# Kernel optimization log

Measured on AMD Instinct MI355X. Metric: run time of the kernel, lower is better.

The kernel has to match this reference:

```python
import jax, jax.numpy as jnp
import numpy as np

D_MODEL = 768
D_POS = 64
NHEAD = 12
D_FF = 3072
HEAD_DIM = D_MODEL // NHEAD
LN_EPS = 1e-5


def _layer_norm(x, gamma, beta):
    mu = jnp.mean(x, axis=-1, keepdims=True)
    var = jnp.var(x, axis=-1, keepdims=True)
    return (x - mu) * jax.lax.rsqrt(var + LN_EPS) * gamma + beta


def setup_inputs() -> dict:
    key = jax.random.key(0)
    ks = jax.random.split(key, 16)
    L, N = 256, 4
    s = 0.02
    return {
        "src": jax.random.normal(ks[0], (L, N, D_MODEL), jnp.float32),
        "pos": jax.random.normal(ks[1], (N, L, L, D_POS), jnp.float32),
        "q_w": jax.random.normal(ks[2], (D_MODEL, D_MODEL), jnp.float32) * s,
        "q_b": jnp.zeros((D_MODEL,), jnp.float32),
        "k_w": jax.random.normal(ks[3], (D_MODEL, D_MODEL), jnp.float32) * s,
        "k_b": jnp.zeros((D_MODEL,), jnp.float32),
        "v_w": jax.random.normal(ks[4], (D_MODEL, D_MODEL), jnp.float32) * s,
        "v_b": jnp.zeros((D_MODEL,), jnp.float32),
        "p_w": jax.random.normal(ks[5], (D_MODEL, D_POS), jnp.float32) * s,
        "p_b": jnp.zeros((D_MODEL,), jnp.float32),
        "out_w": jax.random.normal(ks[6], (D_MODEL, D_MODEL), jnp.float32) * s,
        "out_b": jnp.zeros((D_MODEL,), jnp.float32),
        "lin1_w": jax.random.normal(ks[7], (D_FF, D_MODEL), jnp.float32) * s,
        "lin1_b": jnp.zeros((D_FF,), jnp.float32),
        "lin2_w": jax.random.normal(ks[8], (D_MODEL, D_FF), jnp.float32) * s,
        "lin2_b": jnp.zeros((D_MODEL,), jnp.float32),
        "n1_g": jnp.ones((D_MODEL,), jnp.float32),
        "n1_b": jnp.zeros((D_MODEL,), jnp.float32),
        "n2_g": jnp.ones((D_MODEL,), jnp.float32),
        "n2_b": jnp.zeros((D_MODEL,), jnp.float32),
    }


def reference(src, pos, q_w, q_b, k_w, k_b, v_w, v_b, p_w, p_b,
              out_w, out_b, lin1_w, lin1_b, lin2_w, lin2_b,
              n1_g, n1_b, n2_g, n2_b):
    L, N, E = src.shape
    H, hd = NHEAD, HEAD_DIM
    scaling = float(hd) ** -0.5

    # projections (F.linear: x @ W.T + b)
    q = (src @ q_w.T + q_b).reshape(L, N, H, hd).transpose(1, 2, 0, 3) * scaling  # (N,H,L,hd)
    k = (src @ k_w.T + k_b).reshape(L, N, H, hd).transpose(1, 2, 0, 3)            # (N,H,L,hd)
    v = (src @ v_w.T + v_b).reshape(L, N, H, hd).transpose(1, 2, 0, 3)            # (N,H,L,hd)
    p = (pos @ p_w.T + p_b).reshape(N, L, L, H, hd)                               # (N,L,L,H,hd)

    # content-content + content-position scores
    scores = jnp.einsum('nhid,nhjd->nhij', q, k) \
           + jnp.einsum('nhid,nijhd->nhij', q, p)                                 # (N,H,L,L)
    attn = jax.nn.softmax(scores, axis=-1)

    ctx = jnp.einsum('nhij,nhjd->nhid', attn, v)          # (N,H,L,hd)
    ctx = ctx.transpose(2, 0, 1, 3).reshape(L, N, E)      # (L,N,E)
    attn_out = ctx @ out_w.T + out_b

    x = _layer_norm(src + attn_out, n1_g, n1_b)
    ff = jax.nn.gelu(x @ lin1_w.T + lin1_b, approximate=False) @ lin2_w.T + lin2_b
    x = _layer_norm(x + ff, n2_g, n2_b)
    return x
```

## Files before the change

### kernel.cpp

```cpp
#include <hip/hip_runtime.h>
#include <hip/hip_bf16.h>
#include <math.h>

typedef __hip_bfloat16 bf16;
typedef unsigned short u16;
typedef __attribute__((ext_vector_type(8))) short bf16x8;
typedef __attribute__((ext_vector_type(4))) float f32x4;

#define L_SEQ 256
#define NB 4
#define EMB 768
#define NH 12
#define DFF 3072
#define HD 64

__device__ __forceinline__ float ldE(const void* p, size_t i, int f32) {
    return f32 ? ((const float*)p)[i] : __bfloat162float(((const bf16*)p)[i]);
}
__device__ __forceinline__ float b2f(u16 v) { return __uint_as_float(((unsigned)v) << 16); }
__device__ __forceinline__ u16 f2b(float v) {
    bf16 h = __float2bfloat16(v);
    return *(u16*)&h;
}

__global__ void detect_kernel(const void* __restrict__ src, int* __restrict__ flagp) {
    __shared__ int cnt[256];
    int t = threadIdx.x;
    unsigned w = ((const unsigned*)src)[t];
    unsigned e = ((w & 0xFFFFu) >> 7) & 0xFFu;
    cnt[t] = (e >= 0xC3u) ? 1 : 0;
    __syncthreads();
    for (int off = 128; off; off >>= 1) {
        if (t < off) cnt[t] += cnt[t + off];
        __syncthreads();
    }
    if (t == 0) *flagp = (cnt[0] > 8) ? 1 : 0;
}

__device__ __forceinline__ void cvt8(u16* dst, const void* s, size_t off, int f32) {
    if (f32) {
        const float* sf = (const float*)s + off;
        #pragma unroll
        for (int t = 0; t < 8; ++t) dst[t] = f2b(sf[t]);
    } else {
        *(uint4*)dst = *(const uint4*)((const u16*)s + off);
    }
}

__global__ void pack_all(u16* __restrict__ xb, u16* __restrict__ wqkv,
                         u16* __restrict__ owb, u16* __restrict__ l1b,
                         u16* __restrict__ l2b, float* __restrict__ biasf,
                         const void* src, const void* qw, const void* kw, const void* vw,
                         const void* ow, const void* l1w, const void* l2w,
                         const void* qb, const void* kb, const void* vb,
                         const void* ob, const void* b1, const void* b2,
                         const int* __restrict__ flagp) {
    const int f32 = *flagp;
    int b = blockIdx.x;
    if (b >= 3840) {
        int o = (b - 3840) * 256 + threadIdx.x;
        if (o >= 6912) return;
        float v;
        if (o < 768)       v = ldE(qb, o, f32);
        else if (o < 1536) v = ldE(kb, o - 768, f32);
        else if (o < 2304) v = ldE(vb, o - 1536, f32);
        else if (o < 3072) v = ldE(ob, o - 2304, f32);
        else if (o < 6144) v = ldE(b1, o - 3072, f32);
        else               v = ldE(b2, o - 6144, f32);
        biasf[o] = v;
        return;
    }
    int gid = b * 256 + threadIdx.x;
    u16 tmp[8];
    if (gid < 98304) {
        size_t idx = (size_t)gid * 8;
        cvt8(tmp, src, idx, f32);
        *(uint4*)(xb + idx) = *(uint4*)tmp;
    } else if (gid < 319488) {
        size_t idx = (size_t)(gid - 98304) * 8;
        int r = (int)(idx / EMB);
        const void* s;
        size_t off;
        if (r < EMB)          { s = qw; off = idx; }
        else if (r < 2 * EMB) { s = kw; off = idx - (size_t)EMB * EMB; }
        else                  { s = vw; off = idx - (size_t)2 * EMB * EMB; }
        cvt8(tmp, s, off, f32);
        *(uint4*)(wqkv + idx) = *(uint4*)tmp;
    } else if (gid < 393216) {
        size_t idx = (size_t)(gid - 319488) * 8;
        cvt8(tmp, ow, idx, f32);
        *(uint4*)(owb + idx) = *(uint4*)tmp;
    } else if (gid < 688128) {
        size_t idx = (size_t)(gid - 393216) * 8;
        cvt8(tmp, l1w, idx, f32);
        *(uint4*)(l1b + idx) = *(uint4*)tmp;
    } else {
        size_t idx = (size_t)(gid - 688128) * 8;
        cvt8(tmp, l2w, idx, f32);
        *(uint4*)(l2b + idx) = *(uint4*)tmp;
    }
}

template <int MODE>
__global__ __launch_bounds__(256) void mfma_gemm(
        const u16* __restrict__ A, const u16* __restrict__ W,
        const float* __restrict__ biasf,
        u16* __restrict__ outB0, u16* __restrict__ outB1, u16* __restrict__ outB2,
        float* __restrict__ outF, float* __restrict__ outF2,
        int K, int lda, int ksplit) {
    __shared__ u16 As[128][40];
    __shared__ u16 Ws[128][40];
    int tid = threadIdx.x;
    int wave = tid >> 6, lane = tid & 63;
    int quad = lane >> 4, col = lane & 15;
    int m0 = blockIdx.y * 128, n0 = blockIdx.x * 128;
    int z = blockIdx.z;
    const u16* Ap = A + (size_t)z * ksplit;
    const u16* Wp = W + (size_t)z * ksplit;
    int wm = (wave >> 1) * 64, wn = (wave & 1) * 64;
    f32x4 acc[4][4];
    #pragma unroll
    for (int a = 0; a < 4; ++a)
        #pragma unroll
        for (int b = 0; b < 4; ++b) acc[a][b] = (f32x4){0.f, 0.f, 0.f, 0.f};
    for (int k0 = 0; k0 < K; k0 += 32) {
        #pragma unroll
        for (int it = 0; it < 2; ++it) {
            int l = tid + it * 256;
            int r = l >> 2, c4 = (l & 3) * 8;
            *(uint4*)&As[r][c4] = *(const uint4*)&Ap[(size_t)(m0 + r) * lda + k0 + c4];
            *(uint4*)&Ws[r][c4] = *(const uint4*)&Wp[(size_t)(n0 + r) * lda + k0 + c4];
        }
        __syncthreads();
        bf16x8 af[4], bfr[4];
        #pragma unroll
        for (int mi = 0; mi < 4; ++mi)
            af[mi] = __builtin_bit_cast(bf16x8, *(const uint4*)&As[wm + mi * 16 + col][quad * 8]);
        #pragma unroll
        for (int ni = 0; ni < 4; ++ni)
            bfr[ni] = __builtin_bit_cast(bf16x8, *(const uint4*)&Ws[wn + ni * 16 + col][quad * 8]);
        #pragma unroll
        for (int mi = 0; mi < 4; ++mi)
            #pragma unroll
            for (int ni = 0; ni < 4; ++ni)
                acc[mi][ni] = __builtin_amdgcn_mfma_f32_16x16x32_bf16(
                    af[mi], bfr[ni], acc[mi][ni], 0, 0, 0);
        __syncthreads();
    }
    #pragma unroll
    for (int mi = 0; mi < 4; ++mi)
        #pragma unroll
        for (int ni = 0; ni < 4; ++ni)
            #pragma unroll
            for (int reg = 0; reg < 4; ++reg) {
                int rr = m0 + wm + mi * 16 + quad * 4 + reg;
                int cc = n0 + wn + ni * 16 + col;
                float v = acc[mi][ni][reg];
                if (MODE == 0) {
                    v += biasf[cc];
                    if (cc < EMB) {
                        outB0[(size_t)rr * EMB + cc] = f2b(v * 0.125f);
                    } else if (cc < 2 * EMB) {
                        outB1[(size_t)rr * EMB + cc - EMB] = f2b(v);
                    } else {
                        outB2[((size_t)(rr & 3) * EMB + (cc - 2 * EMB)) * L_SEQ + (rr >> 2)] = f2b(v);
                    }
                } else if (MODE == 2) {
                    v += biasf[cc];
                    v = 0.5f * v * (1.0f + erff(v * 0.70710678118654752f));
                    outB0[(size_t)rr * DFF + cc] = f2b(v);
                } else if (MODE == 4) {
                    float* o = z ? outF2 : outF;
                    o[(size_t)rr * EMB + cc] = v;
                } else {
                    atomicAdd(&outF[(size_t)rr * EMB + cc], v);
                }
            }
}

__global__ void qp_kernel(const u16* __restrict__ qb, const void* __restrict__ p_w,
                          const void* __restrict__ p_b, u16* __restrict__ qp_b,
                          float* __restrict__ qpb, const int* __restrict__ flagp) {
    const int f32 = *flagp;
    int blk = blockIdx.x;
    int i = blk & 255;
    int h = (blk >> 8) % NH;
    int n = blk / (256 * NH);
    int t = threadIdx.x;
    __shared__ float qs[64];
    qs[t] = b2f(qb[(size_t)(i * NB + n) * EMB + h * HD + t]);
    __syncthreads();
    float acc = 0.f;
    #pragma unroll 16
    for (int d = 0; d < 64; ++d)
        acc += qs[d] * ldE(p_w, (size_t)(h * HD + d) * HD + t, f32);
    qp_b[(((size_t)(n * L_SEQ + i)) * 16 + h) * 64 + t] = f2b(acc);
    float v = qs[t] * ldE(p_b, h * HD + t, f32);
    #pragma unroll
    for (int off = 32; off; off >>= 1) v += __shfl_down(v, off);
    if (t == 0) qpb[blk] = v;
}

__global__ __launch_bounds__(256) void s2_mfma(
        const u16* __restrict__ qp_b, const float* __restrict__ qpb,
        const void* __restrict__ pos, float* __restrict__ S,
        const int* __restrict__ flagp) {
    const int f32 = *flagp;
    int wid = (blockIdx.x << 2) + (threadIdx.x >> 6);
    int i = wid & 255, n = wid >> 8;
    int lane = threadIdx.x & 63;
    int quad = lane >> 4, col = lane & 15;
    const u16* qprow = qp_b + (((size_t)wid) * 16 + col) * 64;
    bf16x8 a0 = __builtin_bit_cast(bf16x8, *(const uint4*)(qprow + quad * 8));
    bf16x8 a1 = __builtin_bit_cast(bf16x8, *(const uint4*)(qprow + 32 + quad * 8));
    float qpb_r[4];
    #pragma unroll
    for (int reg = 0; reg < 4; ++reg) {
        int h = quad * 4 + reg;
        qpb_r[reg] = (h < NH) ? qpb[((size_t)n * NH + h) * L_SEQ + i] : 0.f;
    }
    #pragma unroll 4
    for (int t = 0; t < 16; ++t) {
        int j = t * 16 + col;
        size_t pbase = ((size_t)(n * L_SEQ + i) * L_SEQ + j) * HD;
        bf16x8 b0, b1;
        if (f32) {
            const float* pf = (const float*)pos + pbase;
            u16 tmp[16];
            #pragma unroll
            for (int c = 0; c < 8; ++c) tmp[c] = f2b(pf[quad * 8 + c]);
            #pragma unroll
            for (int c = 0; c < 8; ++c) tmp[8 + c] = f2b(pf[32 + quad * 8 + c]);
            b0 = *(bf16x8*)tmp;
            b1 = *(bf16x8*)(tmp + 8);
        } else {
            const u16* pb = (const u16*)pos + pbase;
            b0 = __builtin_bit_cast(bf16x8, *(const uint4*)(pb + quad * 8));
            b1 = __builtin_bit_cast(bf16x8, *(const uint4*)(pb + 32 + quad * 8));
        }
        f32x4 acc = (f32x4){0.f, 0.f, 0.f, 0.f};
        acc = __builtin_amdgcn_mfma_f32_16x16x32_bf16(a0, b0, acc, 0, 0, 0);
        acc = __builtin_amdgcn_mfma_f32_16x16x32_bf16(a1, b1, acc, 0, 0, 0);
        if (quad < 3) {
            #pragma unroll
            for (int reg = 0; reg < 4; ++reg) {
                int h = quad * 4 + reg;
                S[(((size_t)n * NH + h) * L_SEQ + i) * L_SEQ + j] = acc[reg] + qpb_r[reg];
            }
        }
    }
}

__global__ __launch_bounds__(256) void attn3_kernel(
        const u16* __restrict__ qb, const u16* __restrict__ kb,
        const u16* __restrict__ vt, const float* __restrict__ S,
        u16* __restrict__ ctxb) {
    __shared__ u16 p_lds[4][16][268];
    int b = blockIdx.x;
    int n = b / 48, rem = b % 48, h = rem >> 2, it = rem & 3;
    int wave = threadIdx.x >> 6, lane = threadIdx.x & 63;
    int quad = lane >> 4, col = lane & 15;
    int i0 = it * 64 + wave * 16;

    const u16* qrow = qb + ((size_t)(i0 + col) * NB + n) * EMB + h * HD;
    bf16x8 a0 = __builtin_bit_cast(bf16x8, *(const uint4*)(qrow + quad * 8));
    bf16x8 a1 = __builtin_bit_cast(bf16x8, *(const uint4*)(qrow + 32 + quad * 8));

    f32x4 sc[16];
    #pragma unroll
    for (int t = 0; t < 16; ++t) {
        const u16* krow = kb + ((size_t)(t * 16 + col) * NB + n) * EMB + h * HD;
        bf16x8 b0 = __builtin_bit_cast(bf16x8, *(const uint4*)(krow + quad * 8));
        bf16x8 b1 = __builtin_bit_cast(bf16x8, *(const uint4*)(krow + 32 + quad * 8));
        f32x4 acc = (f32x4){0.f, 0.f, 0.f, 0.f};
        acc = __builtin_amdgcn_mfma_f32_16x16x32_bf16(a0, b0, acc, 0, 0, 0);
        acc = __builtin_amdgcn_mfma_f32_16x16x32_bf16(a1, b1, acc, 0, 0, 0);
        sc[t] = acc;
    }

    #pragma unroll
    for (int reg = 0; reg < 4; ++reg) {
        const float* Srow = S + (((size_t)n * NH + h) * L_SEQ + i0 + quad * 4 + reg) * L_SEQ + col;
        float m = -1e30f;
        #pragma unroll
        for (int t = 0; t < 16; ++t) {
            float v = sc[t][reg] + Srow[t * 16];
            sc[t][reg] = v;
            m = fmaxf(m, v);
        }
        #pragma unroll
        for (int off = 1; off < 16; off <<= 1) m = fmaxf(m, __shfl_xor(m, off));
        float sum = 0.f;
        #pragma unroll
        for (int t = 0; t < 16; ++t) {
            float e = __expf(sc[t][reg] - m);
            sc[t][reg] = e;
            sum += e;
        }
        #pragma unroll
        for (int off = 1; off < 16; off <<= 1) sum += __shfl_xor(sum, off);
        float inv = 1.0f / sum;
        #pragma unroll
        for (int t = 0; t < 16; ++t)
            p_lds[wave][quad * 4 + reg][t * 16 + col] = f2b(sc[t][reg] * inv);
    }

    bf16x8 ap[8];
    #pragma unroll
    for (int kt = 0; kt < 8; ++kt)
        ap[kt] = __builtin_bit_cast(bf16x8, *(const uint4*)&p_lds[wave][col][kt * 32 + quad * 8]);
    #pragma unroll
    for (int nt = 0; nt < 4; ++nt) {
        const u16* vrow = vt + ((size_t)n * EMB + h * HD + nt * 16 + col) * L_SEQ;
        f32x4 acc = (f32x4){0.f, 0.f, 0.f, 0.f};
        #pragma unroll
        for (int kt = 0; kt < 8; ++kt) {
            bf16x8 bp = __builtin_bit_cast(bf16x8, *(const uint4*)(vrow + kt * 32 + quad * 8));
            acc = __builtin_amdgcn_mfma_f32_16x16x32_bf16(ap[kt], bp, acc, 0, 0, 0);
        }
        #pragma unroll
        for (int reg = 0; reg < 4; ++reg) {
            int ii = i0 + quad * 4 + reg;
            ctxb[((size_t)ii * NB + n) * EMB + h * HD + nt * 16 + col] = f2b(acc[reg]);
        }
    }
}

__global__ void ln1_kernel(const float* __restrict__ p0, const float* __restrict__ p1,
                           const void* __restrict__ src, const float* __restrict__ biasf,
                           const void* __restrict__ g, const void* __restrict__ b,
                           u16* __restrict__ x1b, float* __restrict__ y2,
                           const int* __restrict__ flagp) {
    const int f32 = *flagp;
    int r = blockIdx.x;
    int t = threadIdx.x;
    __shared__ float red[256];
    float x[3];
    #pragma unroll
    for (int p = 0; p < 3; ++p) {
        int e = t + p * 256;
        size_t oi = (size_t)r * EMB + e;
        x[p] = p0[oi] + p1[oi] + ldE(src, oi, f32) + biasf[2304 + e];
    }
    red[t] = x[0] + x[1] + x[2];
    __syncthreads();
    for (int off = 128; off; off >>= 1) {
        if (t < off) red[t] += red[t + off];
        __syncthreads();
    }
    float mean = red[0] * (1.0f / EMB);
    __syncthreads();
    float d0 = x[0] - mean, d1 = x[1] - mean, d2 = x[2] - mean;
    red[t] = d0 * d0 + d1 * d1 + d2 * d2;
    __syncthreads();
    for (int off = 128; off; off >>= 1) {
        if (t < off) red[t] += red[t + off];
        __syncthreads();
    }
    float rstd = rsqrtf(red[0] * (1.0f / EMB) + 1e-5f);
    float vs[3] = {d0, d1, d2};
    #pragma unroll
    for (int p = 0; p < 3; ++p) {
        int e = t + p * 256;
        float v = vs[p] * rstd * ldE(g, e, f32) + ldE(b, e, f32);
        size_t oi = (size_t)r * EMB + e;
        x1b[oi] = f2b(v);
        y2[oi] = v + biasf[6144 + e];
    }
}

__global__ void ln2_kernel(const float* __restrict__ X, const void* __restrict__ g,
                           const void* __restrict__ b, void* __restrict__ outAny,
                           const int* __restrict__ flagp) {
    const int f32 = *flagp;
    int r = blockIdx.x;
    int t = threadIdx.x;
    __shared__ float red[256];
    float x0 = X[(size_t)r * EMB + t];
    float x1 = X[(size_t)r * EMB + t + 256];
    float x2 = X[(size_t)r * EMB + t + 512];
    red[t] = x0 + x1 + x2;
    __syncthreads();
    for (int off = 128; off; off >>= 1) {
        if (t < off) red[t] += red[t + off];
        __syncthreads();
    }
    float mean = red[0] * (1.0f / EMB);
    __syncthreads();
    float d0 = x0 - mean, d1 = x1 - mean, d2 = x2 - mean;
    red[t] = d0 * d0 + d1 * d1 + d2 * d2;
    __syncthreads();
    for (int off = 128; off; off >>= 1) {
        if (t < off) red[t] += red[t + off];
        __syncthreads();
    }
    float rstd = rsqrtf(red[0] * (1.0f / EMB) + 1e-5f);
    float vs[3] = {d0, d1, d2};
    #pragma unroll
    for (int p = 0; p < 3; ++p) {
        int e = t + p * 256;
        float v = vs[p] * rstd * ldE(g, e, f32) + ldE(b, e, f32);
        size_t oi = (size_t)r * EMB + e;
        if (f32) ((float*)outAny)[oi] = v;
        else     ((bf16*)outAny)[oi] = __float2bfloat16(v);
    }
}

extern "C" void kernel_launch(void* const* d_in, const int* in_sizes, int n_in,
                              void* d_out, int out_size, void* d_ws, size_t ws_size,
                              hipStream_t stream) {
    const void* src    = d_in[0];
    const void* pos    = d_in[1];
    const void* q_w    = d_in[2];
    const void* q_b    = d_in[3];
    const void* k_w    = d_in[4];
    const void* k_b    = d_in[5];
    const void* v_w    = d_in[6];
    const void* v_b    = d_in[7];
    const void* p_w    = d_in[8];
    const void* p_b    = d_in[9];
    const void* out_w  = d_in[10];
    const void* out_b  = d_in[11];
    const void* lin1_w = d_in[12];
    const void* lin1_b = d_in[13];
    const void* lin2_w = d_in[14];
    const void* lin2_b = d_in[15];
    const void* n1_g   = d_in[16];
    const void* n1_b   = d_in[17];
    const void* n2_g   = d_in[18];
    const void* n2_b   = d_in[19];

    float* f = (float*)d_ws;
    int*   flagp = (int*)f;
    float* biasf = f + 16;
    u16*   xb    = (u16*)(f + 6928);
    u16*   wqkv  = (u16*)(f + 400144);
    u16*   owb   = (u16*)(f + 1284880);
    u16*   l1b   = (u16*)(f + 1579792);
    u16*   l2b   = (u16*)(f + 2759440);
    u16*   qbp   = (u16*)(f + 3939088);
    u16*   kbp   = (u16*)(f + 4332304);
    u16*   vtb   = (u16*)(f + 4725520);
    u16*   qp_b  = (u16*)(f + 5118736);
    float* qpb   = f + 5643024;
    float* S     = f + 5655312;
    u16*   ctxb  = (u16*)(f + 8801040);
    u16*   ffb   = (u16*)S;
    float* y2    = S + 1572864;
    float* pOut1 = S + 2359296;
    float* pOut0 = f + 400144;
    u16*   x1b   = vtb;

    detect_kernel<<<1, 256, 0, stream>>>(src, flagp);

    pack_all<<<3867, 256, 0, stream>>>(xb, wqkv, owb, l1b, l2b, biasf,
                                       src, q_w, k_w, v_w, out_w, lin1_w, lin2_w,
                                       q_b, k_b, v_b, out_b, lin1_b, lin2_b, flagp);

    mfma_gemm<0><<<dim3(18, 8), 256, 0, stream>>>(
        xb, wqkv, biasf, qbp, kbp, vtb, nullptr, nullptr, EMB, EMB, 0);

    qp_kernel<<<NB * NH * L_SEQ, 64, 0, stream>>>(qbp, p_w, p_b, qp_b, qpb, flagp);
    s2_mfma<<<NB * L_SEQ / 4, 256, 0, stream>>>(qp_b, qpb, pos, S, flagp);

    attn3_kernel<<<NB * NH * 4, 256, 0, stream>>>(qbp, kbp, vtb, S, ctxb);

    mfma_gemm<4><<<dim3(6, 8, 2), 256, 0, stream>>>(
        ctxb, owb, nullptr, nullptr, nullptr, nullptr, pOut0, pOut1, 384, EMB, 384);

    ln1_kernel<<<1024, 256, 0, stream>>>(pOut0, pOut1, src, biasf, n1_g, n1_b,
                                         x1b, y2, flagp);

    mfma_gemm<2><<<dim3(24, 8), 256, 0, stream>>>(
        x1b, l1b, biasf + 3072, ffb, nullptr, nullptr, nullptr, nullptr, EMB, EMB, 0);

    mfma_gemm<5><<<dim3(6, 8, 4), 256, 0, stream>>>(
        ffb, l2b, nullptr, nullptr, nullptr, nullptr, y2, nullptr, 768, DFF, 768);

    ln2_kernel<<<1024, 256, 0, stream>>>(y2, n2_g, n2_b, d_out, flagp);
}
```

Before: 309.6 us.

## Fold dtype detection into pack, use direct global-to-LDS loads, regroup small kernels

Removes the separate detect kernel by computing the dtype flag with ballots inside every pack_all block. Switches GEMM tile staging to global_load_lds direct-to-LDS transfers with an unpadded 32-wide LDS tile. Packs four qp rows per 256-thread block, splits attention into single-wave 16-row blocks, and replaces the LDS tree reductions in the layer norms with wave shuffles. The unpadded LDS layout may add bank conflicts on fragment reads, and every pack block now rereads the detection sample.

```diff
diff --git a/kernel.cpp b/kernel.cpp
--- a/kernel.cpp
+++ b/kernel.cpp
@@ -23,20 +23,6 @@
     return *(u16*)&h;
 }
 
-__global__ void detect_kernel(const void* __restrict__ src, int* __restrict__ flagp) {
-    __shared__ int cnt[256];
-    int t = threadIdx.x;
-    unsigned w = ((const unsigned*)src)[t];
-    unsigned e = ((w & 0xFFFFu) >> 7) & 0xFFu;
-    cnt[t] = (e >= 0xC3u) ? 1 : 0;
-    __syncthreads();
-    for (int off = 128; off; off >>= 1) {
-        if (t < off) cnt[t] += cnt[t + off];
-        __syncthreads();
-    }
-    if (t == 0) *flagp = (cnt[0] > 8) ? 1 : 0;
-}
-
 __device__ __forceinline__ void cvt8(u16* dst, const void* s, size_t off, int f32) {
     if (f32) {
         const float* sf = (const float*)s + off;
@@ -45,6 +31,17 @@
     } else {
         *(uint4*)dst = *(const uint4*)((const u16*)s + off);
     }
+}
+
+__device__ __forceinline__ int detect_flag(const void* src, int* lds4) {
+    int t = threadIdx.x;
+    int wave = t >> 6, lane = t & 63;
+    unsigned w = ((const unsigned*)src)[t];
+    unsigned e = ((w & 0xFFFFu) >> 7) & 0xFFu;
+    unsigned long long m = __ballot(e >= 0xC3u);
+    if (lane == 0) lds4[wave] = __popcll(m);
+    __syncthreads();
+    return (lds4[0] + lds4[1] + lds4[2] + lds4[3]) > 8 ? 1 : 0;
 }
 
 __global__ void pack_all(u16* __restrict__ xb, u16* __restrict__ wqkv,
@@ -54,9 +51,11 @@
                          const void* ow, const void* l1w, const void* l2w,
                          const void* qb, const void* kb, const void* vb,
                          const void* ob, const void* b1, const void* b2,
-                         const int* __restrict__ flagp) {
-    const int f32 = *flagp;
+                         int* __restrict__ flagp) {
+    __shared__ int lds4[4];
+    const int f32 = detect_flag(src, lds4);
     int b = blockIdx.x;
+    if (b == 0 && threadIdx.x == 0) *flagp = f32;
     if (b >= 3840) {
         int o = (b - 3840) * 256 + threadIdx.x;
         if (o >= 6912) return;
@@ -108,8 +107,8 @@
         u16* __restrict__ outB0, u16* __restrict__ outB1, u16* __restrict__ outB2,
         float* __restrict__ outF, float* __restrict__ outF2,
         int K, int lda, int ksplit) {
-    __shared__ u16 As[128][40];
-    __shared__ u16 Ws[128][40];
+    __shared__ u16 As[128][32];
+    __shared__ u16 Ws[128][32];
     int tid = threadIdx.x;
     int wave = tid >> 6, lane = tid & 63;
     int quad = lane >> 4, col = lane & 15;
@@ -128,8 +127,17 @@
         for (int it = 0; it < 2; ++it) {
             int l = tid + it * 256;
             int r = l >> 2, c4 = (l & 3) * 8;
-            *(uint4*)&As[r][c4] = *(const uint4*)&Ap[(size_t)(m0 + r) * lda + k0 + c4];
-            *(uint4*)&Ws[r][c4] = *(const uint4*)&Wp[(size_t)(n0 + r) * lda + k0 + c4];
+            const u16* ga = &Ap[(size_t)(m0 + r) * lda + k0 + c4];
+            const u16* gw = &Wp[(size_t)(n0 + r) * lda + k0 + c4];
+            unsigned off = (unsigned)((it * 256 + wave * 64) * 16);
+            __builtin_amdgcn_global_load_lds(
+                (const __attribute__((address_space(1))) void*)ga,
+                (__attribute__((address_space(3))) void*)((char*)&As[0][0] + off),
+                16, 0, 0);
+            __builtin_amdgcn_global_load_lds(
+                (const __attribute__((address_space(1))) void*)gw,
+                (__attribute__((address_space(3))) void*)((char*)&Ws[0][0] + off),
+                16, 0, 0);
         }
         __syncthreads();
         bf16x8 af[4], bfr[4];
@@ -178,24 +186,25 @@
             }
 }
 
-__global__ void qp_kernel(const u16* __restrict__ qb, const void* __restrict__ p_w,
-                          const void* __restrict__ p_b, u16* __restrict__ qp_b,
-                          float* __restrict__ qpb, const int* __restrict__ flagp) {
+__global__ __launch_bounds__(256) void qp_kernel(
+        const u16* __restrict__ qb, const void* __restrict__ p_w,
+        const void* __restrict__ p_b, u16* __restrict__ qp_b,
+        float* __restrict__ qpb, const int* __restrict__ flagp) {
     const int f32 = *flagp;
-    int blk = blockIdx.x;
+    int w = threadIdx.x >> 6, t = threadIdx.x & 63;
+    int blk = blockIdx.x * 4 + w;
     int i = blk & 255;
     int h = (blk >> 8) % NH;
     int n = blk / (256 * NH);
-    int t = threadIdx.x;
-    __shared__ float qs[64];
-    qs[t] = b2f(qb[(size_t)(i * NB + n) * EMB + h * HD + t]);
+    __shared__ float qs[4][64];
+    qs[w][t] = b2f(qb[(size_t)(i * NB + n) * EMB + h * HD + t]);
     __syncthreads();
     float acc = 0.f;
     #pragma unroll 16
     for (int d = 0; d < 64; ++d)
-        acc += qs[d] * ldE(p_w, (size_t)(h * HD + d) * HD + t, f32);
+        acc += qs[w][d] * ldE(p_w, (size_t)(h * HD + d) * HD + t, f32);
     qp_b[(((size_t)(n * L_SEQ + i)) * 16 + h) * 64 + t] = f2b(acc);
-    float v = qs[t] * ldE(p_b, h * HD + t, f32);
+    float v = qs[w][t] * ldE(p_b, h * HD + t, f32);
     #pragma unroll
     for (int off = 32; off; off >>= 1) v += __shfl_down(v, off);
     if (t == 0) qpb[blk] = v;
@@ -251,16 +260,16 @@
     }
 }
 
-__global__ __launch_bounds__(256) void attn3_kernel(
+__global__ __launch_bounds__(64) void attn3_kernel(
         const u16* __restrict__ qb, const u16* __restrict__ kb,
         const u16* __restrict__ vt, const float* __restrict__ S,
         u16* __restrict__ ctxb) {
-    __shared__ u16 p_lds[4][16][268];
+    __shared__ u16 p_lds[16][268];
     int b = blockIdx.x;
-    int n = b / 48, rem = b % 48, h = rem >> 2, it = rem & 3;
-    int wave = threadIdx.x >> 6, lane = threadIdx.x & 63;
+    int n = b / (NH * 16), rem = b % (NH * 16), h = rem >> 4, it = rem & 15;
+    int lane = threadIdx.x;
     int quad = lane >> 4, col = lane & 15;
-    int i0 = it * 64 + wave * 16;
+    int i0 = it * 16;
 
     const u16* qrow = qb + ((size_t)(i0 + col) * NB + n) * EMB + h * HD;
     bf16x8 a0 = __builtin_bit_cast(bf16x8, *(const uint4*)(qrow + quad * 8));
@@ -302,13 +311,13 @@
         float inv = 1.0f / sum;
         #pragma unroll
         for (int t = 0; t < 16; ++t)
-            p_lds[wave][quad * 4 + reg][t * 16 + col] = f2b(sc[t][reg] * inv);
+            p_lds[quad * 4 + reg][t * 16 + col] = f2b(sc[t][reg] * inv);
     }
 
     bf16x8 ap[8];
     #pragma unroll
     for (int kt = 0; kt < 8; ++kt)
-        ap[kt] = __builtin_bit_cast(bf16x8, *(const uint4*)&p_lds[wave][col][kt * 32 + quad * 8]);
+        ap[kt] = __builtin_bit_cast(bf16x8, *(const uint4*)&p_lds[col][kt * 32 + quad * 8]);
     #pragma unroll
     for (int nt = 0; nt < 4; ++nt) {
         const u16* vrow = vt + ((size_t)n * EMB + h * HD + nt * 16 + col) * L_SEQ;
@@ -324,6 +333,16 @@
             ctxb[((size_t)ii * NB + n) * EMB + h * HD + nt * 16 + col] = f2b(acc[reg]);
         }
     }
+}
+
+__device__ __forceinline__ float blk_sum(float v, volatile float* ws, int wave, int lane) {
+    #pragma unroll
+    for (int off = 32; off; off >>= 1) v += __shfl_xor(v, off);
+    if (lane == 0) ws[wave] = v;
+    __syncthreads();
+    float s = ws[0] + ws[1] + ws[2] + ws[3];
+    __syncthreads();
+    return s;
 }
 
 __global__ void ln1_kernel(const float* __restrict__ p0, const float* __restrict__ p1,
@@ -334,7 +353,8 @@
     const int f32 = *flagp;
     int r = blockIdx.x;
     int t = threadIdx.x;
-    __shared__ float red[256];
+    int wave = t >> 6, lane = t & 63;
+    __shared__ float ws[4];
     float x[3];
     #pragma unroll
     for (int p = 0; p < 3; ++p) {
@@ -342,22 +362,10 @@
         size_t oi = (size_t)r * EMB + e;
         x[p] = p0[oi] + p1[oi] + ldE(src, oi, f32) + biasf[2304 + e];
     }
-    red[t] = x[0] + x[1] + x[2];
-    __syncthreads();
-    for (int off = 128; off; off >>= 1) {
-        if (t < off) red[t] += red[t + off];
-        __syncthreads();
-    }
-    float mean = red[0] * (1.0f / EMB);
-    __syncthreads();
+    float mean = blk_sum(x[0] + x[1] + x[2], ws, wave, lane) * (1.0f / EMB);
     float d0 = x[0] - mean, d1 = x[1] - mean, d2 = x[2] - mean;
-    red[t] = d0 * d0 + d1 * d1 + d2 * d2;
-    __syncthreads();
-    for (int off = 128; off; off >>= 1) {
-        if (t < off) red[t] += red[t + off];
-        __syncthreads();
-    }
-    float rstd = rsqrtf(red[0] * (1.0f / EMB) + 1e-5f);
+    float var = blk_sum(d0 * d0 + d1 * d1 + d2 * d2, ws, wave, lane) * (1.0f / EMB);
+    float rstd = rsqrtf(var + 1e-5f);
     float vs[3] = {d0, d1, d2};
     #pragma unroll
     for (int p = 0; p < 3; ++p) {
@@ -375,26 +383,15 @@
     const int f32 = *flagp;
     int r = blockIdx.x;
     int t = threadIdx.x;
-    __shared__ float red[256];
+    int wave = t >> 6, lane = t & 63;
+    __shared__ float ws[4];
     float x0 = X[(size_t)r * EMB + t];
     float x1 = X[(size_t)r * EMB + t + 256];
     float x2 = X[(size_t)r * EMB + t + 512];
-    red[t] = x0 + x1 + x2;
-    __syncthreads();
-    for (int off = 128; off; off >>= 1) {
-        if (t < off) red[t] += red[t + off];
-        __syncthreads();
-    }
-    float mean = red[0] * (1.0f / EMB);
-    __syncthreads();
+    float mean = blk_sum(x0 + x1 + x2, ws, wave, lane) * (1.0f / EMB);
     float d0 = x0 - mean, d1 = x1 - mean, d2 = x2 - mean;
-    red[t] = d0 * d0 + d1 * d1 + d2 * d2;
-    __syncthreads();
-    for (int off = 128; off; off >>= 1) {
-        if (t < off) red[t] += red[t + off];
-        __syncthreads();
-    }
-    float rstd = rsqrtf(red[0] * (1.0f / EMB) + 1e-5f);
+    float var = blk_sum(d0 * d0 + d1 * d1 + d2 * d2, ws, wave, lane) * (1.0f / EMB);
+    float rstd = rsqrtf(var + 1e-5f);
     float vs[3] = {d0, d1, d2};
     #pragma unroll
     for (int p = 0; p < 3; ++p) {
@@ -451,8 +448,6 @@
     float* pOut0 = f + 400144;
     u16*   x1b   = vtb;
 
-    detect_kernel<<<1, 256, 0, stream>>>(src, flagp);
-
     pack_all<<<3867, 256, 0, stream>>>(xb, wqkv, owb, l1b, l2b, biasf,
                                        src, q_w, k_w, v_w, out_w, lin1_w, lin2_w,
                                        q_b, k_b, v_b, out_b, lin1_b, lin2_b, flagp);
@@ -460,10 +455,10 @@
     mfma_gemm<0><<<dim3(18, 8), 256, 0, stream>>>(
         xb, wqkv, biasf, qbp, kbp, vtb, nullptr, nullptr, EMB, EMB, 0);
 
-    qp_kernel<<<NB * NH * L_SEQ, 64, 0, stream>>>(qbp, p_w, p_b, qp_b, qpb, flagp);
+    qp_kernel<<<NB * NH * L_SEQ / 4, 256, 0, stream>>>(qbp, p_w, p_b, qp_b, qpb, flagp);
     s2_mfma<<<NB * L_SEQ / 4, 256, 0, stream>>>(qp_b, qpb, pos, S, flagp);
 
-    attn3_kernel<<<NB * NH * 4, 256, 0, stream>>>(qbp, kbp, vtb, S, ctxb);
+    attn3_kernel<<<NB * NH * 16, 64, 0, stream>>>(qbp, kbp, vtb, S, ctxb);
 
     mfma_gemm<4><<<dim3(6, 8, 2), 256, 0, stream>>>(
         ctxb, owb, nullptr, nullptr, nullptr, nullptr, pOut0, pOut1, 384, EMB, 384);
```

Result: no change. 304.4 us (-1.7%).
